# Kernel tuning notes

Hardware: AMD Instinct MI355X
Metric: run time of the kernel (lower is better)

Reference implementation:

```python
import jax, jax.numpy as jnp
import numpy as np

DIM = 1024
NUM_HEADS = 16
HEAD_DIM = DIM // NUM_HEADS
SCALE = HEAD_DIM ** -0.5


def setup_inputs() -> dict:
    key = jax.random.key(0)
    ks = jax.random.split(key, 5)
    B, N = 2, 2048
    x = jax.random.normal(ks[0], (B, N, DIM), dtype=jnp.float32)
    # nn.Linear weights: stored as [out, in]; we keep that convention.
    w_qkv = jax.random.normal(ks[1], (3 * DIM, DIM), dtype=jnp.float32) * (DIM ** -0.5)
    b_qkv = jax.random.normal(ks[2], (3 * DIM,), dtype=jnp.float32) * 0.02
    w_proj = jax.random.normal(ks[3], (DIM, DIM), dtype=jnp.float32) * (DIM ** -0.5)
    b_proj = jax.random.normal(ks[4], (DIM,), dtype=jnp.float32) * 0.02
    return {"x": x, "w_qkv": w_qkv, "b_qkv": b_qkv, "w_proj": w_proj, "b_proj": b_proj}


def reference(x, w_qkv, b_qkv, w_proj, b_proj):
    B, N, C = x.shape
    H, D = NUM_HEADS, HEAD_DIM
    qkv = x @ w_qkv.T + b_qkv                      # [B, N, 3C]
    qkv = qkv.reshape(B, N, 3, H, D)
    q = qkv[:, :, 0].transpose(0, 2, 1, 3)         # [B, H, N, D]
    k = qkv[:, :, 1].transpose(0, 2, 1, 3)
    v = qkv[:, :, 2].transpose(0, 2, 1, 3)
    attn = jnp.einsum("bhnd,bhmd->bhnm", q, k) * SCALE  # [B, H, N, N]
    attn = jax.nn.softmax(attn, axis=-1)
    out = jnp.einsum("bhnm,bhmd->bhnd", attn, v)   # [B, H, N, D]
    out = out.transpose(0, 2, 1, 3).reshape(B, N, C)
    return out @ w_proj.T + b_proj
```

## Files before the change

### kernel.cpp

```cpp
#include <hip/hip_runtime.h>
#include <math.h>

#define DIMC   1024
#define NHEADS 16
#define HDIM   64
#define BATCH  2
#define SEQ    2048

#define MTOT   (BATCH * SEQ)
#define QKVN   (3 * DIMC)
#define QKVSZ  ((size_t)BATCH * NHEADS * SEQ * HDIM)
#define HEADEL ((size_t)SEQ * HDIM)

#define QSCALE 0.18033688011112042f

typedef __attribute__((ext_vector_type(8))) short bf16x8;
typedef __attribute__((ext_vector_type(4))) short bf16x4;
typedef __attribute__((ext_vector_type(4))) float f32x4;

static __device__ inline short f2bf(float f) {
    union { float f; unsigned u; } v; v.f = f;
    unsigned r = v.u + 0x7fffu + ((v.u >> 16) & 1u);
    return (short)(r >> 16);
}

static __device__ inline unsigned cvt_pk_bf16(float lo, float hi) {
    unsigned r;
    asm("v_cvt_pk_bf16_f32 %0, %1, %2" : "=v"(r) : "v"(lo), "v"(hi));
    return r;
}

#if __has_builtin(__builtin_amdgcn_exp2f)
#define EXP2F(x) __builtin_amdgcn_exp2f(x)
#else
#define EXP2F(x) exp2f(x)
#endif

#define NXB  (MTOT * DIMC / 2048)
#define NWQB (QKVN * DIMC / 2048)
#define NWPB (DIMC * DIMC / 2048)

__global__ __launch_bounds__(256) void cast_all(
    const float* __restrict__ x,  const float* __restrict__ wq,
    const float* __restrict__ wp, short* __restrict__ xb,
    short* __restrict__ wqb, short* __restrict__ wpb)
{
    const float* in; short* out; int base;
    int bid = blockIdx.x;
    if (bid < NXB)              { in = x;  out = xb;  base = bid; }
    else if (bid < NXB + NWQB)  { in = wq; out = wqb; base = bid - NXB; }
    else                        { in = wp; out = wpb; base = bid - NXB - NWQB; }
    int i = (base * 256 + threadIdx.x) * 8;
    float4 a = *(const float4*)&in[i];
    float4 b = *(const float4*)&in[i + 4];
    bf16x8 o;
    o[0] = f2bf(a.x); o[1] = f2bf(a.y); o[2] = f2bf(a.z); o[3] = f2bf(a.w);
    o[4] = f2bf(b.x); o[5] = f2bf(b.y); o[6] = f2bf(b.z); o[7] = f2bf(b.w);
    *(bf16x8*)&out[i] = o;
}

__device__ __forceinline__ void gload16(const void* g, void* l) {
    __builtin_amdgcn_global_load_lds(
        (const __attribute__((address_space(1))) unsigned*)g,
        (__attribute__((address_space(3))) unsigned*)l, 16, 0, 0);
}

#define BAR() do { __builtin_amdgcn_s_barrier(); \
                   __builtin_amdgcn_sched_barrier(0); } while (0)
#define VWAIT8() asm volatile("s_waitcnt vmcnt(8)" ::: "memory")
#define VWAIT0() asm volatile("s_waitcnt vmcnt(0)" ::: "memory")

__device__ __forceinline__ void stage_panel(const short* __restrict__ src,
                                            int row0, int k0,
                                            short* dst, int tid)
{
#pragma unroll
    for (int u = 0; u < 2; ++u) {
        const int gidx = u * 512 + tid;
        const int rl   = gidx >> 3;
        const int cc   = gidx & 7;
        gload16(&src[(size_t)(row0 + rl) * 1024 + k0 + ((cc ^ (rl & 7)) << 3)],
                &dst[(size_t)gidx << 3]);
    }
}

__device__ __forceinline__ void load_b(const short* Bs, int wn, int nh,
                                       int lid, int quad, bf16x8 (&bfr)[2][2])
{
#pragma unroll
    for (int j2 = 0; j2 < 2; ++j2) {
        const int rb = wn + (nh * 2 + j2) * 16 + lid;
#pragma unroll
        for (int kk = 0; kk < 2; ++kk)
            bfr[j2][kk] = *(const bf16x8*)
                &Bs[rb * 64 + (((kk * 4 + quad) ^ (rb & 7)) << 3)];
    }
}

template<int MH>
__device__ __forceinline__ void half_compute(
    const short* As, int wm, int lid, int quad,
    const bf16x8 (&b0)[2][2], const bf16x8 (&b1)[2][2],
    f32x4 (&acc)[8][4])
{
    bf16x8 af[4][2];
#pragma unroll
    for (int i2 = 0; i2 < 4; ++i2) {
        const int r = wm + (MH * 4 + i2) * 16 + lid;
#pragma unroll
        for (int kk = 0; kk < 2; ++kk)
            af[i2][kk] = *(const bf16x8*)
                &As[r * 64 + (((kk * 4 + quad) ^ (r & 7)) << 3)];
    }
    __builtin_amdgcn_s_setprio(1);
#pragma unroll
    for (int i2 = 0; i2 < 4; ++i2)
#pragma unroll
        for (int kk = 0; kk < 2; ++kk) {
            acc[MH * 4 + i2][0] = __builtin_amdgcn_mfma_f32_16x16x32_bf16(
                af[i2][kk], b0[0][kk], acc[MH * 4 + i2][0], 0, 0, 0);
            acc[MH * 4 + i2][1] = __builtin_amdgcn_mfma_f32_16x16x32_bf16(
                af[i2][kk], b0[1][kk], acc[MH * 4 + i2][1], 0, 0, 0);
            acc[MH * 4 + i2][2] = __builtin_amdgcn_mfma_f32_16x16x32_bf16(
                af[i2][kk], b1[0][kk], acc[MH * 4 + i2][2], 0, 0, 0);
            acc[MH * 4 + i2][3] = __builtin_amdgcn_mfma_f32_16x16x32_bf16(
                af[i2][kk], b1[1][kk], acc[MH * 4 + i2][3], 0, 0, 0);
        }
    __builtin_amdgcn_s_setprio(0);
}

__global__ __launch_bounds__(512, 2) void qkv_mfma(
    const short* __restrict__ xb,
    const short* __restrict__ wb,
    const float* __restrict__ bias,
    short* __restrict__ qkvb)
{
    extern __shared__ short lds[];

    const int tid = threadIdx.x;
    const int T  = (blockIdx.x & 7) * 24 + (blockIdx.x >> 3);
    const int m0 = (T / 12) * 256;
    const int j0 = (T % 12) * 256;

    const int lane = tid & 63;
    const int w    = tid >> 6;
    const int quad = lane >> 4;
    const int lid  = lane & 15;
    const int wm = (w >> 2) * 128;
    const int wn = (w & 3) * 64;

    f32x4 acc[8][4];
#pragma unroll
    for (int i = 0; i < 8; ++i)
#pragma unroll
        for (int j = 0; j < 4; ++j) acc[i][j] = (f32x4){0.f, 0.f, 0.f, 0.f};

    stage_panel(xb, m0,       0, lds,                 tid);
    stage_panel(xb, m0 + 128, 0, lds + 8192,          tid);
    stage_panel(wb, j0,       0, lds + 32768,         tid);
    stage_panel(wb, j0 + 128, 0, lds + 32768 + 8192,  tid);

#pragma unroll 2
    for (int kt = 0; kt < 15; ++kt) {
        const int cb = (kt & 1) << 14;
        const int nb = (~kt & 1) << 14;
        const int k1 = (kt + 1) << 6;
        const short* Ac = lds + cb;
        const short* Bc = lds + 32768 + cb;
        short* An = lds + nb;
        short* Bn = lds + 32768 + nb;

        stage_panel(xb, m0,       k1, An,        tid);
        stage_panel(xb, m0 + 128, k1, An + 8192, tid);
        stage_panel(wb, j0,       k1, Bn,        tid);
        stage_panel(wb, j0 + 128, k1, Bn + 8192, tid);

        VWAIT8(); BAR();
        {
            bf16x8 b0[2][2], b1[2][2];
            load_b(Bc, wn, 0, lid, quad, b0);
            load_b(Bc, wn, 1, lid, quad, b1);
            half_compute<0>(Ac, wm, lid, quad, b0, b1, acc);
            half_compute<1>(Ac, wm, lid, quad, b0, b1, acc);
        }
        BAR();
    }
    {
        const short* Ac = lds + 16384;
        const short* Bc = lds + 32768 + 16384;
        VWAIT0(); BAR();
        bf16x8 b0[2][2], b1[2][2];
        load_b(Bc, wn, 0, lid, quad, b0);
        load_b(Bc, wn, 1, lid, quad, b1);
        half_compute<0>(Ac, wm, lid, quad, b0, b1, acc);
        half_compute<1>(Ac, wm, lid, quad, b0, b1, acc);
    }

    const int s = j0 >> 10;

    if (s == 0) {
#pragma unroll
        for (int jb = 0; jb < 4; ++jb) {
            const int jj = j0 + wn + jb * 16 + lid;
            const int hh = (jj & 1023) >> 6;
            const int dd = jj & 63;
            const float bv = bias[jj];
#pragma unroll
            for (int i = 0; i < 8; ++i)
#pragma unroll
                for (int r = 0; r < 4; ++r) {
                    const int mrow = m0 + wm + i * 16 + quad * 4 + r;
                    const int b_ = mrow >> 11, nn = mrow & 2047;
                    qkvb[((size_t)(b_ * NHEADS + hh) * SEQ + nn) * HDIM + dd] =
                        f2bf((acc[i][jb][r] + bv) * QSCALE);
                }
        }
    } else if (s == 1) {
#pragma unroll
        for (int jb = 0; jb < 4; ++jb) {
            const int jj = j0 + wn + jb * 16 + lid;
            const int hh = (jj & 1023) >> 6;
            const int dd = jj & 63;
            const int c2 = dd >> 5;
            const int qd = (dd >> 3) & 3;
            const int jo = dd & 7;
            const float bv = bias[jj];
#pragma unroll
            for (int i = 0; i < 8; ++i) {
                const int mrow0 = m0 + wm + i * 16;
                const int b_ = mrow0 >> 11;
                const int n0 = mrow0 & 2047;
                const int t32 = n0 >> 5;
                const int i16 = (n0 >> 4) & 1;
                const int c = quad & 1;
                const int lidb = (i16 * 2 + (quad >> 1)) * 4;
                size_t base = QKVSZ + (size_t)(b_ * NHEADS + hh) * HEADEL +
                              (size_t)(t32 * 4 + c2 * 2 + c) * 512 +
                              (qd * 16 + lidb) * 8 + jo;
#pragma unroll
                for (int r = 0; r < 4; ++r)
                    qkvb[base + r * 8] = f2bf(acc[i][jb][r] + bv);
            }
        }
    } else {
#pragma unroll
        for (int jb = 0; jb < 4; ++jb) {
            const int jj = j0 + wn + jb * 16 + lid;
            const int hh = (jj & 1023) >> 6;
            const int dd = jj & 63;
            const int fb = dd >> 4;
            const int dl = dd & 15;
            const float bv = bias[jj];
#pragma unroll
            for (int i = 0; i < 8; ++i) {
                const int mrow0 = m0 + wm + i * 16 + quad * 4;
                const int b_ = mrow0 >> 11, n0 = mrow0 & 2047;
                const int t32 = n0 >> 5;
                const int i16 = (n0 >> 4) & 1;
                const int quadpp = i16 * 2 + (quad >> 1);
                bf16x4 o;
#pragma unroll
                for (int r = 0; r < 4; ++r) o[r] = f2bf(acc[i][jb][r] + bv);
                *(bf16x4*)&qkvb[2 * QKVSZ + (size_t)(b_ * NHEADS + hh) * HEADEL +
                                (size_t)(t32 * 4 + fb) * 512 +
                                (quadpp * 16 + dl) * 8 + (quad & 1) * 4] = o;
            }
        }
    }
}

__global__ __launch_bounds__(256, 2) void attn_mfma(
    const short* __restrict__ qkvb,
    short* __restrict__ aob)
{
    __shared__ float Osm[4][4][4][64];
    __shared__ float Lsm[3][64];

    const int tid  = threadIdx.x;
    const int sp   = tid >> 6;
    const int lane = tid & 63;
    const int quad = lane >> 4;
    const int lid  = lane & 15;

    const int bid  = blockIdx.x;
    const int xcd  = bid & 7;
    const int slot = bid >> 3;
    const int pair = xcd * 4 + (slot >> 5);
    const int qblk = slot & 31;
    const int h = pair & 15;
    const int b = pair >> 4;
    const int qbase = qblk * 64;

    const short* Qh = qkvb + (size_t)(b * NHEADS + h) * HEADEL;
    const short* Kf = Qh + QKVSZ;
    const short* Vf = qkvb + 2 * QKVSZ + (size_t)(b * NHEADS + h) * HEADEL;

    bf16x8 bQ[4][2];
#pragma unroll
    for (int g = 0; g < 4; ++g)
#pragma unroll
        for (int c = 0; c < 2; ++c)
            bQ[g][c] = *(const bf16x8*)&Qh[(size_t)(qbase + g * 16 + lid) * HDIM +
                                           c * 32 + quad * 8];

    f32x4 O[4][4];
    f32x4 L[4];
#pragma unroll
    for (int g = 0; g < 4; ++g) {
        L[g] = (f32x4){0.f, 0.f, 0.f, 0.f};
#pragma unroll
        for (int fb = 0; fb < 4; ++fb) O[g][fb] = (f32x4){0.f, 0.f, 0.f, 0.f};
    }
    const bf16x8 ones8 = {(short)0x3F80, (short)0x3F80, (short)0x3F80, (short)0x3F80,
                          (short)0x3F80, (short)0x3F80, (short)0x3F80, (short)0x3F80};

#pragma unroll 2
    for (int cc = 0; cc < SEQ / 128; ++cc) {
        const int t = sp * (SEQ / 128) + cc;
        bf16x8 aK[2][2];
#pragma unroll
        for (int c = 0; c < 2; ++c)
#pragma unroll
            for (int c2 = 0; c2 < 2; ++c2)
                aK[c][c2] = *(const bf16x8*)&Kf[(size_t)(t * 4 + c2 * 2 + c) * 512 +
                                                lane * 8];
        bf16x8 aV[4];
#pragma unroll
        for (int fb = 0; fb < 4; ++fb)
            aV[fb] = *(const bf16x8*)&Vf[(size_t)(t * 4 + fb) * 512 + lane * 8];

#pragma unroll
        for (int g = 0; g < 4; ++g) {
            f32x4 s0 = (f32x4){0.f, 0.f, 0.f, 0.f};
            f32x4 s1 = (f32x4){0.f, 0.f, 0.f, 0.f};
            __builtin_amdgcn_s_setprio(1);
            s0 = __builtin_amdgcn_mfma_f32_16x16x32_bf16(aK[0][0], bQ[g][0], s0, 0, 0, 0);
            s1 = __builtin_amdgcn_mfma_f32_16x16x32_bf16(aK[1][0], bQ[g][0], s1, 0, 0, 0);
            s0 = __builtin_amdgcn_mfma_f32_16x16x32_bf16(aK[0][1], bQ[g][1], s0, 0, 0, 0);
            s1 = __builtin_amdgcn_mfma_f32_16x16x32_bf16(aK[1][1], bQ[g][1], s1, 0, 0, 0);
            __builtin_amdgcn_s_setprio(0);
            union { unsigned u[4]; bf16x8 v; } P;
            P.u[0] = cvt_pk_bf16(EXP2F(s0[0]), EXP2F(s0[1]));
            P.u[1] = cvt_pk_bf16(EXP2F(s0[2]), EXP2F(s0[3]));
            P.u[2] = cvt_pk_bf16(EXP2F(s1[0]), EXP2F(s1[1]));
            P.u[3] = cvt_pk_bf16(EXP2F(s1[2]), EXP2F(s1[3]));
            __builtin_amdgcn_s_setprio(1);
            L[g] = __builtin_amdgcn_mfma_f32_16x16x32_bf16(ones8, P.v, L[g], 0, 0, 0);
#pragma unroll
            for (int fb = 0; fb < 4; ++fb)
                O[g][fb] = __builtin_amdgcn_mfma_f32_16x16x32_bf16(
                    aV[fb], P.v, O[g][fb], 0, 0, 0);
            __builtin_amdgcn_s_setprio(0);
        }
    }

    if (sp != 0 && quad == 0)
#pragma unroll
        for (int g = 0; g < 4; ++g) Lsm[sp - 1][g * 16 + lid] = L[g][0];

    if (sp == 1) {
#pragma unroll
        for (int g = 0; g < 4; ++g)
#pragma unroll
            for (int fb = 0; fb < 4; ++fb)
#pragma unroll
                for (int r = 0; r < 4; ++r)
                    Osm[g][fb][r][lane] = O[g][fb][r];
    }
    __syncthreads();
    if (sp == 0) {
#pragma unroll
        for (int g = 0; g < 4; ++g)
#pragma unroll
            for (int fb = 0; fb < 4; ++fb)
#pragma unroll
                for (int r = 0; r < 4; ++r)
                    O[g][fb][r] += Osm[g][fb][r][lane];
    }
    __syncthreads();
    if (sp == 3) {
#pragma unroll
        for (int g = 0; g < 4; ++g)
#pragma unroll
            for (int fb = 0; fb < 4; ++fb)
#pragma unroll
                for (int r = 0; r < 4; ++r)
                    Osm[g][fb][r][lane] = O[g][fb][r];
    }
    __syncthreads();
    if (sp == 2) {
#pragma unroll
        for (int g = 0; g < 4; ++g)
#pragma unroll
            for (int fb = 0; fb < 4; ++fb)
#pragma unroll
                for (int r = 0; r < 4; ++r)
                    O[g][fb][r] += Osm[g][fb][r][lane];
    }
    __syncthreads();
    if (sp == 2) {
#pragma unroll
        for (int g = 0; g < 4; ++g)
#pragma unroll
            for (int fb = 0; fb < 4; ++fb)
#pragma unroll
                for (int r = 0; r < 4; ++r)
                    Osm[g][fb][r][lane] = O[g][fb][r];
    }
    __syncthreads();
    if (sp == 0) {
#pragma unroll
        for (int g = 0; g < 4; ++g) {
            const float lt = L[g][0] + Lsm[0][g * 16 + lid] +
                             Lsm[1][g * 16 + lid] + Lsm[2][g * 16 + lid];
            const float inv = 1.f / lt;
            const int n = qbase + g * 16 + lid;
            size_t base = ((size_t)(b * SEQ + n)) * DIMC + h * HDIM;
#pragma unroll
            for (int fb = 0; fb < 4; ++fb) {
                bf16x4 o;
#pragma unroll
                for (int r = 0; r < 4; ++r)
                    o[r] = f2bf((O[g][fb][r] + Osm[g][fb][r][lane]) * inv);
                *(bf16x4*)&aob[base + fb * 16 + quad * 4] = o;
            }
        }
    }
}

__global__ __launch_bounds__(256, 2) void proj_mfma(
    const short* __restrict__ ab,
    const short* __restrict__ wb,
    const float* __restrict__ bias,
    float* __restrict__ out)
{
    __shared__ __attribute__((aligned(16))) short Asm[2 * 64 * 32];
    __shared__ __attribute__((aligned(16))) short Bsm[2 * 128 * 32];

    const int tid = threadIdx.x;
    const int m0 = blockIdx.y * 64;
    const int j0 = blockIdx.x * 128;

    const int lane = tid & 63;
    const int w    = tid >> 6;
    const int quad = lane >> 4;
    const int lid  = lane & 15;
    const int wm = (w >> 1) * 32, wn = (w & 1) * 64;

    const int srow = lane >> 2;
    const int skc  = (lane & 3) * 8;

    f32x4 acc[2][4];
#pragma unroll
    for (int i = 0; i < 2; ++i)
#pragma unroll
        for (int j = 0; j < 4; ++j) acc[i][j] = (f32x4){0.f, 0.f, 0.f, 0.f};

    for (int k0 = 0; k0 < 1024; k0 += 64) {
        __syncthreads();
#pragma unroll
        for (int u = 0; u < 2; ++u) {
            const int combo = w * 2 + u;
            const int hh = combo >> 2, rb = combo & 3;
            const int row = rb * 16 + srow;
            gload16(&ab[(size_t)(m0 + row) * 1024 + k0 + hh * 32 + skc],
                    &Asm[hh * 2048 + row * 32 + skc]);
        }
#pragma unroll
        for (int u = 0; u < 4; ++u) {
            const int combo = w * 4 + u;
            const int hh = combo >> 3, rb = combo & 7;
            const int row = rb * 16 + srow;
            gload16(&wb[(size_t)(j0 + row) * 1024 + k0 + hh * 32 + skc],
                    &Bsm[hh * 4096 + row * 32 + skc]);
        }
        __syncthreads();

#pragma unroll
        for (int hh = 0; hh < 2; ++hh) {
            bf16x8 af[2], bfr[4];
#pragma unroll
            for (int i = 0; i < 2; ++i)
                af[i] = *(const bf16x8*)&Asm[hh * 2048 + (wm + i * 16 + lid) * 32 + quad * 8];
#pragma unroll
            for (int j = 0; j < 4; ++j)
                bfr[j] = *(const bf16x8*)&Bsm[hh * 4096 + (wn + j * 16 + lid) * 32 + quad * 8];
#pragma unroll
            for (int i = 0; i < 2; ++i)
#pragma unroll
                for (int j = 0; j < 4; ++j)
                    acc[i][j] = __builtin_amdgcn_mfma_f32_16x16x32_bf16(
                        af[i], bfr[j], acc[i][j], 0, 0, 0);
        }
    }

#pragma unroll
    for (int jb = 0; jb < 4; ++jb) {
        const int jj = j0 + wn + jb * 16 + lid;
        const float bv = bias[jj];
#pragma unroll
        for (int i = 0; i < 2; ++i)
#pragma unroll
            for (int r = 0; r < 4; ++r) {
                const int mrow = m0 + wm + i * 16 + quad * 4 + r;
                out[(size_t)mrow * DIMC + jj] = acc[i][jb][r] + bv;
            }
    }
}

extern "C" void kernel_launch(void* const* d_in, const int* in_sizes, int n_in,
                              void* d_out, int out_size, void* d_ws, size_t ws_size,
                              hipStream_t stream) {
    const float* x      = (const float*)d_in[0];
    const float* w_qkv  = (const float*)d_in[1];
    const float* b_qkv  = (const float*)d_in[2];
    const float* w_proj = (const float*)d_in[3];
    const float* b_proj = (const float*)d_in[4];
    float* out = (float*)d_out;

    short* qkvb   = (short*)d_ws;
    short* xb     = qkvb + 3 * QKVSZ;
    short* wqkvb  = xb + (size_t)MTOT * DIMC;
    short* wprojb = wqkvb + (size_t)QKVN * DIMC;
    short* aob    = wprojb + (size_t)DIMC * DIMC;

    hipFuncSetAttribute((const void*)qkv_mfma,
                        hipFuncAttributeMaxDynamicSharedMemorySize, 131072);

    cast_all<<<NXB + NWQB + NWPB, 256, 0, stream>>>(x, w_qkv, w_proj,
                                                    xb, wqkvb, wprojb);

    qkv_mfma<<<192, 512, 131072, stream>>>(xb, wqkvb, b_qkv, qkvb);

    attn_mfma<<<BATCH * NHEADS * (SEQ / 64), 256, 0, stream>>>(qkvb, aob);

    dim3 g3(DIMC / 128, MTOT / 64);
    proj_mfma<<<g3, 256, 0, stream>>>(aob, wprojb, b_proj, out);
}
```

Measured before the change: 172.5 us.

## Shrink QKV GEMM tiles to 128x128 and double-buffer K/V register loads in attention

The QKV projection GEMM moves from 256x256 tiles with 512 threads and 128KB of dynamic LDS to 128x128 tiles with 256 threads and 64KB of static LDS, launching 768 blocks instead of 192. This spreads the work over more blocks so all CUs stay busy and lowers LDS use per block, at the cost of less operand reuse per loaded tile. Separately, the attention loop now software-pipelines its K/V fragment loads into two register sets, prefetching the next chunk while the current one is computed. That pipelining raises register pressure.

Measured after the change: 167.5 us (median of 3 runs). 1.03x faster.

```diff
diff --git a/kernel.cpp b/kernel.cpp
--- a/kernel.cpp
+++ b/kernel.cpp
@@ -70,13 +70,13 @@
 #define VWAIT8() asm volatile("s_waitcnt vmcnt(8)" ::: "memory")
 #define VWAIT0() asm volatile("s_waitcnt vmcnt(0)" ::: "memory")
 
-__device__ __forceinline__ void stage_panel(const short* __restrict__ src,
-                                            int row0, int k0,
-                                            short* dst, int tid)
-{
-#pragma unroll
-    for (int u = 0; u < 2; ++u) {
-        const int gidx = u * 512 + tid;
+__device__ __forceinline__ void stage_panel128(const short* __restrict__ src,
+                                               int row0, int k0,
+                                               short* dst, int tid)
+{
+#pragma unroll
+    for (int u = 0; u < 4; ++u) {
+        const int gidx = u * 256 + tid;
         const int rl   = gidx >> 3;
         const int cc   = gidx & 7;
         gload16(&src[(size_t)(row0 + rl) * 1024 + k0 + ((cc ^ (rl & 7)) << 3)],
@@ -84,81 +84,63 @@
     }
 }
 
-__device__ __forceinline__ void load_b(const short* Bs, int wn, int nh,
-                                       int lid, int quad, bf16x8 (&bfr)[2][2])
-{
-#pragma unroll
-    for (int j2 = 0; j2 < 2; ++j2) {
-        const int rb = wn + (nh * 2 + j2) * 16 + lid;
+__device__ __forceinline__ void tile_compute(
+    const short* Ac, const short* Bc, int wm, int wn,
+    int lid, int quad, f32x4 (&acc)[4][4])
+{
+    bf16x8 bfr[4][2];
+#pragma unroll
+    for (int j2 = 0; j2 < 4; ++j2) {
+        const int rb = wn + j2 * 16 + lid;
 #pragma unroll
         for (int kk = 0; kk < 2; ++kk)
             bfr[j2][kk] = *(const bf16x8*)
-                &Bs[rb * 64 + (((kk * 4 + quad) ^ (rb & 7)) << 3)];
-    }
-}
-
-template<int MH>
-__device__ __forceinline__ void half_compute(
-    const short* As, int wm, int lid, int quad,
-    const bf16x8 (&b0)[2][2], const bf16x8 (&b1)[2][2],
-    f32x4 (&acc)[8][4])
-{
-    bf16x8 af[4][2];
+                &Bc[rb * 64 + (((kk * 4 + quad) ^ (rb & 7)) << 3)];
+    }
 #pragma unroll
     for (int i2 = 0; i2 < 4; ++i2) {
-        const int r = wm + (MH * 4 + i2) * 16 + lid;
-#pragma unroll
-        for (int kk = 0; kk < 2; ++kk)
-            af[i2][kk] = *(const bf16x8*)
-                &As[r * 64 + (((kk * 4 + quad) ^ (r & 7)) << 3)];
-    }
-    __builtin_amdgcn_s_setprio(1);
-#pragma unroll
-    for (int i2 = 0; i2 < 4; ++i2)
-#pragma unroll
-        for (int kk = 0; kk < 2; ++kk) {
-            acc[MH * 4 + i2][0] = __builtin_amdgcn_mfma_f32_16x16x32_bf16(
-                af[i2][kk], b0[0][kk], acc[MH * 4 + i2][0], 0, 0, 0);
-            acc[MH * 4 + i2][1] = __builtin_amdgcn_mfma_f32_16x16x32_bf16(
-                af[i2][kk], b0[1][kk], acc[MH * 4 + i2][1], 0, 0, 0);
-            acc[MH * 4 + i2][2] = __builtin_amdgcn_mfma_f32_16x16x32_bf16(
-                af[i2][kk], b1[0][kk], acc[MH * 4 + i2][2], 0, 0, 0);
-            acc[MH * 4 + i2][3] = __builtin_amdgcn_mfma_f32_16x16x32_bf16(
-                af[i2][kk], b1[1][kk], acc[MH * 4 + i2][3], 0, 0, 0);
-        }
-    __builtin_amdgcn_s_setprio(0);
-}
-
-__global__ __launch_bounds__(512, 2) void qkv_mfma(
+        const int r = wm + i2 * 16 + lid;
+        bf16x8 a0 = *(const bf16x8*)&Ac[r * 64 + (((quad) ^ (r & 7)) << 3)];
+        bf16x8 a1 = *(const bf16x8*)&Ac[r * 64 + (((4 + quad) ^ (r & 7)) << 3)];
+        __builtin_amdgcn_s_setprio(1);
+#pragma unroll
+        for (int j2 = 0; j2 < 4; ++j2) {
+            acc[i2][j2] = __builtin_amdgcn_mfma_f32_16x16x32_bf16(
+                a0, bfr[j2][0], acc[i2][j2], 0, 0, 0);
+            acc[i2][j2] = __builtin_amdgcn_mfma_f32_16x16x32_bf16(
+                a1, bfr[j2][1], acc[i2][j2], 0, 0, 0);
+        }
+        __builtin_amdgcn_s_setprio(0);
+    }
+}
+
+__global__ __launch_bounds__(256, 2) void qkv_mfma(
     const short* __restrict__ xb,
     const short* __restrict__ wb,
     const float* __restrict__ bias,
     short* __restrict__ qkvb)
 {
-    extern __shared__ short lds[];
+    __shared__ __attribute__((aligned(16))) short lds[2 * 16384];
 
     const int tid = threadIdx.x;
-    const int T  = (blockIdx.x & 7) * 24 + (blockIdx.x >> 3);
-    const int m0 = (T / 12) * 256;
-    const int j0 = (T % 12) * 256;
+    const int T  = (blockIdx.x & 7) * 96 + (blockIdx.x >> 3);
+    const int m0 = (T / 24) * 128;
+    const int j0 = (T % 24) * 128;
 
     const int lane = tid & 63;
     const int w    = tid >> 6;
     const int quad = lane >> 4;
     const int lid  = lane & 15;
-    const int wm = (w >> 2) * 128;
-    const int wn = (w & 3) * 64;
-
-    f32x4 acc[8][4];
-#pragma unroll
-    for (int i = 0; i < 8; ++i)
+    const int wm = (w >> 1) * 64, wn = (w & 1) * 64;
+
+    f32x4 acc[4][4];
+#pragma unroll
+    for (int i = 0; i < 4; ++i)
 #pragma unroll
         for (int j = 0; j < 4; ++j) acc[i][j] = (f32x4){0.f, 0.f, 0.f, 0.f};
 
-    stage_panel(xb, m0,       0, lds,                 tid);
-    stage_panel(xb, m0 + 128, 0, lds + 8192,          tid);
-    stage_panel(wb, j0,       0, lds + 32768,         tid);
-    stage_panel(wb, j0 + 128, 0, lds + 32768 + 8192,  tid);
+    stage_panel128(xb, m0, 0, lds,        tid);
+    stage_panel128(wb, j0, 0, lds + 8192, tid);
 
 #pragma unroll 2
     for (int kt = 0; kt < 15; ++kt) {
@@ -166,34 +148,19 @@
         const int nb = (~kt & 1) << 14;
         const int k1 = (kt + 1) << 6;
         const short* Ac = lds + cb;
-        const short* Bc = lds + 32768 + cb;
-        short* An = lds + nb;
-        short* Bn = lds + 32768 + nb;
-
-        stage_panel(xb, m0,       k1, An,        tid);
-        stage_panel(xb, m0 + 128, k1, An + 8192, tid);
-        stage_panel(wb, j0,       k1, Bn,        tid);
-        stage_panel(wb, j0 + 128, k1, Bn + 8192, tid);
+        const short* Bc = Ac + 8192;
+
+        stage_panel128(xb, m0, k1, lds + nb,        tid);
+        stage_panel128(wb, j0, k1, lds + nb + 8192, tid);
 
         VWAIT8(); BAR();
-        {
-            bf16x8 b0[2][2], b1[2][2];
-            load_b(Bc, wn, 0, lid, quad, b0);
-            load_b(Bc, wn, 1, lid, quad, b1);
-            half_compute<0>(Ac, wm, lid, quad, b0, b1, acc);
-            half_compute<1>(Ac, wm, lid, quad, b0, b1, acc);
-        }
+        tile_compute(Ac, Bc, wm, wn, lid, quad, acc);
         BAR();
     }
     {
         const short* Ac = lds + 16384;
-        const short* Bc = lds + 32768 + 16384;
         VWAIT0(); BAR();
-        bf16x8 b0[2][2], b1[2][2];
-        load_b(Bc, wn, 0, lid, quad, b0);
-        load_b(Bc, wn, 1, lid, quad, b1);
-        half_compute<0>(Ac, wm, lid, quad, b0, b1, acc);
-        half_compute<1>(Ac, wm, lid, quad, b0, b1, acc);
+        tile_compute(Ac, Ac + 8192, wm, wn, lid, quad, acc);
     }
 
     const int s = j0 >> 10;
@@ -206,7 +173,7 @@
             const int dd = jj & 63;
             const float bv = bias[jj];
 #pragma unroll
-            for (int i = 0; i < 8; ++i)
+            for (int i = 0; i < 4; ++i)
 #pragma unroll
                 for (int r = 0; r < 4; ++r) {
                     const int mrow = m0 + wm + i * 16 + quad * 4 + r;
@@ -226,7 +193,7 @@
             const int jo = dd & 7;
             const float bv = bias[jj];
 #pragma unroll
-            for (int i = 0; i < 8; ++i) {
+            for (int i = 0; i < 4; ++i) {
                 const int mrow0 = m0 + wm + i * 16;
                 const int b_ = mrow0 >> 11;
                 const int n0 = mrow0 & 2047;
@@ -252,7 +219,7 @@
             const int dl = dd & 15;
             const float bv = bias[jj];
 #pragma unroll
-            for (int i = 0; i < 8; ++i) {
+            for (int i = 0; i < 4; ++i) {
                 const int mrow0 = m0 + wm + i * 16 + quad * 4;
                 const int b_ = mrow0 >> 11, n0 = mrow0 & 2047;
                 const int t32 = n0 >> 5;
@@ -266,6 +233,51 @@
                                 (quadpp * 16 + dl) * 8 + (quad & 1) * 4] = o;
             }
         }
+    }
+}
+
+__device__ __forceinline__ void load_kv(
+    const short* __restrict__ Kf, const short* __restrict__ Vf,
+    int t, int lane, bf16x8 (&aK)[2][2], bf16x8 (&aV)[4])
+{
+#pragma unroll
+    for (int c = 0; c < 2; ++c)
+#pragma unroll
+        for (int c2 = 0; c2 < 2; ++c2)
+            aK[c][c2] = *(const bf16x8*)&Kf[(size_t)(t * 4 + c2 * 2 + c) * 512 +
+                                            lane * 8];
+#pragma unroll
+    for (int fb = 0; fb < 4; ++fb)
+        aV[fb] = *(const bf16x8*)&Vf[(size_t)(t * 4 + fb) * 512 + lane * 8];
+}
+
+__device__ __forceinline__ void attn_chunk(
+    const bf16x8 (&aK)[2][2], const bf16x8 (&aV)[4],
+    const bf16x8 (&bQ)[4][2], const bf16x8& ones8,
+    f32x4 (&O)[4][4], f32x4 (&L)[4])
+{
+#pragma unroll
+    for (int g = 0; g < 4; ++g) {
+        f32x4 s0 = (f32x4){0.f, 0.f, 0.f, 0.f};
+        f32x4 s1 = (f32x4){0.f, 0.f, 0.f, 0.f};
+        __builtin_amdgcn_s_setprio(1);
+        s0 = __builtin_amdgcn_mfma_f32_16x16x32_bf16(aK[0][0], bQ[g][0], s0, 0, 0, 0);
+        s1 = __builtin_amdgcn_mfma_f32_16x16x32_bf16(aK[1][0], bQ[g][0], s1, 0, 0, 0);
+        s0 = __builtin_amdgcn_mfma_f32_16x16x32_bf16(aK[0][1], bQ[g][1], s0, 0, 0, 0);
+        s1 = __builtin_amdgcn_mfma_f32_16x16x32_bf16(aK[1][1], bQ[g][1], s1, 0, 0, 0);
+        __builtin_amdgcn_s_setprio(0);
+        union { unsigned u[4]; bf16x8 v; } P;
+        P.u[0] = cvt_pk_bf16(EXP2F(s0[0]), EXP2F(s0[1]));
+        P.u[1] = cvt_pk_bf16(EXP2F(s0[2]), EXP2F(s0[3]));
+        P.u[2] = cvt_pk_bf16(EXP2F(s1[0]), EXP2F(s1[1]));
+        P.u[3] = cvt_pk_bf16(EXP2F(s1[2]), EXP2F(s1[3]));
+        __builtin_amdgcn_s_setprio(1);
+        L[g] = __builtin_amdgcn_mfma_f32_16x16x32_bf16(ones8, P.v, L[g], 0, 0, 0);
+#pragma unroll
+        for (int fb = 0; fb < 4; ++fb)
+            O[g][fb] = __builtin_amdgcn_mfma_f32_16x16x32_bf16(
+                aV[fb], P.v, O[g][fb], 0, 0, 0);
+        __builtin_amdgcn_s_setprio(0);
     }
 }
 
@@ -314,44 +326,16 @@
     const bf16x8 ones8 = {(short)0x3F80, (short)0x3F80, (short)0x3F80, (short)0x3F80,
                           (short)0x3F80, (short)0x3F80, (short)0x3F80, (short)0x3F80};
 
+    bf16x8 aK0[2][2], aV0[4], aK1[2][2], aV1[4];
+    const int t0 = sp * (SEQ / 128);
+    load_kv(Kf, Vf, t0, lane, aK0, aV0);
 #pragma unroll 2
-    for (int cc = 0; cc < SEQ / 128; ++cc) {
-        const int t = sp * (SEQ / 128) + cc;
-        bf16x8 aK[2][2];
-#pragma unroll
-        for (int c = 0; c < 2; ++c)
-#pragma unroll
-            for (int c2 = 0; c2 < 2; ++c2)
-                aK[c][c2] = *(const bf16x8*)&Kf[(size_t)(t * 4 + c2 * 2 + c) * 512 +
-                                                lane * 8];
-        bf16x8 aV[4];
-#pragma unroll
-        for (int fb = 0; fb < 4; ++fb)
-            aV[fb] = *(const bf16x8*)&Vf[(size_t)(t * 4 + fb) * 512 + lane * 8];
-
-#pragma unroll
-        for (int g = 0; g < 4; ++g) {
-            f32x4 s0 = (f32x4){0.f, 0.f, 0.f, 0.f};
-            f32x4 s1 = (f32x4){0.f, 0.f, 0.f, 0.f};
-            __builtin_amdgcn_s_setprio(1);
-            s0 = __builtin_amdgcn_mfma_f32_16x16x32_bf16(aK[0][0], bQ[g][0], s0, 0, 0, 0);
-            s1 = __builtin_amdgcn_mfma_f32_16x16x32_bf16(aK[1][0], bQ[g][0], s1, 0, 0, 0);
-            s0 = __builtin_amdgcn_mfma_f32_16x16x32_bf16(aK[0][1], bQ[g][1], s0, 0, 0, 0);
-            s1 = __builtin_amdgcn_mfma_f32_16x16x32_bf16(aK[1][1], bQ[g][1], s1, 0, 0, 0);
-            __builtin_amdgcn_s_setprio(0);
-            union { unsigned u[4]; bf16x8 v; } P;
-            P.u[0] = cvt_pk_bf16(EXP2F(s0[0]), EXP2F(s0[1]));
-            P.u[1] = cvt_pk_bf16(EXP2F(s0[2]), EXP2F(s0[3]));
-            P.u[2] = cvt_pk_bf16(EXP2F(s1[0]), EXP2F(s1[1]));
-            P.u[3] = cvt_pk_bf16(EXP2F(s1[2]), EXP2F(s1[3]));
-            __builtin_amdgcn_s_setprio(1);
-            L[g] = __builtin_amdgcn_mfma_f32_16x16x32_bf16(ones8, P.v, L[g], 0, 0, 0);
-#pragma unroll
-            for (int fb = 0; fb < 4; ++fb)
-                O[g][fb] = __builtin_amdgcn_mfma_f32_16x16x32_bf16(
-                    aV[fb], P.v, O[g][fb], 0, 0, 0);
-            __builtin_amdgcn_s_setprio(0);
-        }
+    for (int cc = 0; cc < 16; cc += 2) {
+        load_kv(Kf, Vf, t0 + cc + 1, lane, aK1, aV1);
+        attn_chunk(aK0, aV0, bQ, ones8, O, L);
+        if (cc + 2 < 16)
+            load_kv(Kf, Vf, t0 + cc + 2, lane, aK0, aV0);
+        attn_chunk(aK1, aV1, bQ, ones8, O, L);
     }
 
     if (sp != 0 && quad == 0)
@@ -524,13 +508,10 @@
     short* wprojb = wqkvb + (size_t)QKVN * DIMC;
     short* aob    = wprojb + (size_t)DIMC * DIMC;
 
-    hipFuncSetAttribute((const void*)qkv_mfma,
-                        hipFuncAttributeMaxDynamicSharedMemorySize, 131072);
-
     cast_all<<<NXB + NWQB + NWPB, 256, 0, stream>>>(x, w_qkv, w_proj,
                                                     xb, wqkvb, wprojb);
 
-    qkv_mfma<<<192, 512, 131072, stream>>>(xb, wqkvb, b_qkv, qkvb);
+    qkv_mfma<<<768, 256, 0, stream>>>(xb, wqkvb, b_qkv, qkvb);
 
     attn_mfma<<<BATCH * NHEADS * (SEQ / 64), 256, 0, stream>>>(qkvb, aob);
 
```
